# Optimization experiments

Measured on AMD Instinct MI355X. Metric: run time of the kernel, lower is better.

## Reference

```python
import jax, jax.numpy as jnp
import numpy as np
from jax import lax

B, T, C = 2, 2048, 1024
HEAD = 64          # head_size N
H = C // HEAD      # n_head
EPS_GN = 0.00064   # GroupNorm epsilon from module


def l2norm(x, eps=1e-12):
    inv = lax.rsqrt(jnp.sum(x * x, axis=-1, keepdims=True) + eps)
    return x * jnp.maximum(inv, eps)


def group_norm(x, gamma, beta, groups, eps):
    n, c = x.shape
    xg = x.reshape(n, groups, c // groups)
    mu = jnp.mean(xg, axis=-1, keepdims=True)
    var = jnp.mean(jnp.square(xg - mu), axis=-1, keepdims=True)
    xg = (xg - mu) * lax.rsqrt(var + eps)
    return xg.reshape(n, c) * gamma + beta


def rwkv7_scan(r, w, k, v, a, b):
    # all [B,T,H,N]; w is log-decay, actual per-channel decay = exp(-exp(w))
    decay = jnp.exp(-jnp.exp(w))

    def step(state, inp):  # state: [B,H,N,N] (value dim i, key dim j)
        r_t, d_t, k_t, v_t, a_t, b_t = inp  # each [B,H,N]
        sa = jnp.einsum('bhij,bhj->bhi', state, a_t)
        state = (state * d_t[:, :, None, :]
                 + sa[:, :, :, None] * b_t[:, :, None, :]
                 + v_t[:, :, :, None] * k_t[:, :, None, :])
        out = jnp.einsum('bhij,bhj->bhi', state, r_t)
        return state, out

    xs = tuple(jnp.moveaxis(t, 1, 0) for t in (r, decay, k, v, a, b))
    state0 = jnp.zeros((r.shape[0], H, HEAD, HEAD), r.dtype)
    final_state, out = lax.scan(step, state0, xs)
    return jnp.moveaxis(out, 0, 1), final_state


def setup_inputs():
    key = jax.random.key(0)
    ks = jax.random.split(key, 32)

    def p(i, shape, scale=0.02):
        return jax.random.normal(ks[i], shape, jnp.float32) * scale

    return dict(
        x=jax.random.normal(ks[0], (B, T, C), jnp.float32),
        v_first=jax.random.normal(ks[1], (B, T, C), jnp.float32),
        x_r=p(2, (1, 1, C)), x_w=p(3, (1, 1, C)), x_k=p(4, (1, 1, C)),
        x_v=p(5, (1, 1, C)), x_a=p(6, (1, 1, C)), x_g=p(7, (1, 1, C)),
        w0=p(8, (1, 1, C)), w1=p(9, (C, 64)), w2=p(10, (64, C)),
        a0=p(11, (1, 1, C)), a1=p(12, (C, 64)), a2=p(13, (64, C)),
        v0=p(14, (1, 1, C)), v1=p(15, (C, 32)), v2=p(16, (32, C)),
        g1=p(17, (C, 128)), g2=p(18, (128, C)),
        k_k=p(19, (1, 1, C), 0.5), k_a=p(20, (1, 1, C), 0.5),
        r_k=p(21, (H, HEAD), 0.5),
        Wr=p(22, (C, C)), Wk=p(23, (C, C)), Wv=p(24, (C, C)), Wo=p(25, (C, C)),
        ln_gamma=jnp.ones((C,), jnp.float32),
        ln_beta=jnp.zeros((C,), jnp.float32),
    )


def reference(x, v_first, x_r, x_w, x_k, x_v, x_a, x_g, w0, w1, w2,
              a0, a1, a2, v0, v1, v2, g1, g2, k_k, k_a, r_k,
              Wr, Wk, Wv, Wo, ln_gamma, ln_beta):
    # time_shift(x) - x
    xx = jnp.pad(x, ((0, 0), (1, 0), (0, 0)))[:, :-1] - x
    xr = x + xx * x_r
    xw = x + xx * x_w
    xk = x + xx * x_k
    xv = x + xx * x_v
    xa = x + xx * x_a
    xg = x + xx * x_g

    r = xr @ Wr
    k = xk @ Wk
    v = xv @ Wv
    w = -jax.nn.softplus(-(w0 + jnp.tanh(xw @ w1) @ w2)) - 0.5
    # v_first provided (non-first layer path)
    v = v + (v_first - v) * jax.nn.sigmoid(v0 + (xv @ v1) @ v2)
    a = jax.nn.sigmoid(a0 + (xa @ a1) @ a2)
    g = jax.nn.sigmoid(xg @ g1) @ g2

    kk = l2norm((k * k_k).reshape(B, T, H, HEAD)).reshape(B, T, C)
    k = k * (1.0 + (a - 1.0) * k_a)

    r4 = r.reshape(B, T, H, HEAD)
    y, _ = rwkv7_scan(r4,
                      w.reshape(B, T, H, HEAD),
                      k.reshape(B, T, H, HEAD),
                      v.reshape(B, T, H, HEAD),
                      (-kk).reshape(B, T, H, HEAD),
                      (kk * a).reshape(B, T, H, HEAD))

    y = group_norm(y.reshape(B * T, C), ln_gamma, ln_beta, H, EPS_GN).reshape(B, T, C)

    k4 = k.reshape(B, T, H, HEAD)
    v4 = v.reshape(B, T, H, HEAD)
    rwkv = jnp.sum(r4 * k4 * r_k, axis=-1, keepdims=True) * v4  # [B,T,H,N]
    y = y + rwkv.reshape(B, T, C)
    return (y * g) @ Wo
```

## Files before the change

### kernel.cpp

```cpp
#include <hip/hip_runtime.h>
#include <hip/hip_bf16.h>
#include <math.h>

#define TSEQ 2048
#define HEADS 16
#define HSZ 64
#define CDIM 1024
#define MROWS 4096
#define CHUNK 64
#define NCHUNK (TSEQ/CHUNK)
#define NBH 32
#define LSTR 68
#define K2 2048

typedef short bf16x8 __attribute__((ext_vector_type(8)));
typedef short bf16x4 __attribute__((ext_vector_type(4)));
typedef float f32x4 __attribute__((ext_vector_type(4)));

__device__ __forceinline__ float sigf(float x) { return 1.0f / (1.0f + expf(-x)); }

__device__ __forceinline__ short to_bf16(float f) {
    __hip_bfloat16 h = __float2bfloat16(f);
    return *reinterpret_cast<short*>(&h);
}
__device__ __forceinline__ float bf2f(short s) {
    unsigned int u = ((unsigned int)(unsigned short)s) << 16;
    return __uint_as_float(u);
}

__global__ __launch_bounds__(256)
void mix_make(const float* __restrict__ x, short* __restrict__ ax)
{
    const int m = blockIdx.x;
    const int cc = threadIdx.x * 4;
    const float4 xv = *(const float4*)(x + (size_t)m*CDIM + cc);
    float4 xp = make_float4(0.f, 0.f, 0.f, 0.f);
    if ((m & (TSEQ-1)) != 0) xp = *(const float4*)(x + (size_t)(m-1)*CDIM + cc);
    bf16x4 a, b;
    a[0] = to_bf16(xv.x); a[1] = to_bf16(xv.y);
    a[2] = to_bf16(xv.z); a[3] = to_bf16(xv.w);
    b[0] = to_bf16(xp.x - xv.x); b[1] = to_bf16(xp.y - xv.y);
    b[2] = to_bf16(xp.z - xv.z); b[3] = to_bf16(xp.w - xv.w);
    *(bf16x4*)(ax + (size_t)m*K2 + cc)        = a;
    *(bf16x4*)(ax + (size_t)m*K2 + CDIM + cc) = b;
}

__global__ __launch_bounds__(256)
void transpose_cvt(const float* __restrict__ W, short* __restrict__ Wt,
                   const int K, const int N)
{
    __shared__ float t[32][33];
    const int k0 = blockIdx.y * 32, n0 = blockIdx.x * 32;
    const int lx = threadIdx.x & 31, ly = threadIdx.x >> 5;
#pragma unroll
    for (int i = 0; i < 4; ++i)
        t[ly + i*8][lx] = W[(size_t)(k0 + ly + i*8)*N + n0 + lx];
    __syncthreads();
#pragma unroll
    for (int i = 0; i < 4; ++i)
        Wt[(size_t)(n0 + ly + i*8)*K + k0 + lx] = to_bf16(t[lx][ly + i*8]);
}

__global__ __launch_bounds__(256)
void transpose_cvt_scaled(const float* __restrict__ W, const float* __restrict__ mix,
                          short* __restrict__ Wt, const int N)
{
    __shared__ float t[32][33];
    const int k0 = blockIdx.y * 32, n0 = blockIdx.x * 32;
    const int lx = threadIdx.x & 31, ly = threadIdx.x >> 5;
#pragma unroll
    for (int i = 0; i < 4; ++i)
        t[ly + i*8][lx] = W[(size_t)(k0 + ly + i*8)*N + n0 + lx];
    __syncthreads();
    const float mv = mix[k0 + lx];
#pragma unroll
    for (int i = 0; i < 4; ++i) {
        const float w = t[lx][ly + i*8];
        short* base = Wt + (size_t)(n0 + ly + i*8)*K2 + k0 + lx;
        base[0]    = to_bf16(w);
        base[CDIM] = to_bf16(mv * w);
    }
}

template<int BN, int MODE>
__global__ __launch_bounds__(256)
void gemm_mfma(const short* __restrict__ A, const short* __restrict__ Bt,
               void* __restrict__ Cptr, const int M, const int N, const int K)
{
    constexpr int BM = 128, BK = 32;
    constexpr int ASTR = BK + 8;
    constexpr int NWC = (BN >= 128) ? 2 : 1;
    constexpr int NWR = 4 / NWC;
    constexpr int WM = BM / NWR;
    constexpr int WN = BN / NWC;
    constexpr int AM = WM / 16;
    constexpr int AN = WN / 16;

    __shared__ short As[BM * ASTR];
    __shared__ short Bs[BN * ASTR];

    const int tid  = threadIdx.x;
    const int bm   = blockIdx.y * BM;
    const int bn   = blockIdx.x * BN;
    const int wid  = tid >> 6;
    const int lane = tid & 63;
    const int wr   = wid / NWC;
    const int wc   = wid % NWC;
    const int lrow = lane & 15;
    const int koff = (lane >> 4) * 8;

    f32x4 acc[AM][AN];
#pragma unroll
    for (int m = 0; m < AM; ++m)
#pragma unroll
        for (int n = 0; n < AN; ++n)
            acc[m][n] = (f32x4){0.f, 0.f, 0.f, 0.f};

    for (int k0 = 0; k0 < K; k0 += BK) {
        __syncthreads();
#pragma unroll
        for (int p = 0; p < (BM*BK)/(256*8); ++p) {
            const int c = p*256 + tid;
            const int row = c >> 2;
            const int kc  = (c & 3) * 8;
            *(bf16x8*)&As[row*ASTR + kc] =
                *(const bf16x8*)(A + (size_t)(bm+row)*K + k0 + kc);
        }
        {
            constexpr int CHUNKS = (BN*BK)/8;
#pragma unroll
            for (int p = 0; p < (CHUNKS + 255)/256; ++p) {
                const int c = p*256 + tid;
                if ((CHUNKS & 255) == 0 || c < CHUNKS) {
                    const int col = c >> 2;
                    const int kc  = (c & 3) * 8;
                    *(bf16x8*)&Bs[col*ASTR + kc] =
                        *(const bf16x8*)(Bt + (size_t)(bn+col)*K + k0 + kc);
                }
            }
        }
        __syncthreads();

        bf16x8 af[AM], bfv[AN];
#pragma unroll
        for (int m = 0; m < AM; ++m)
            af[m] = *(const bf16x8*)&As[(wr*WM + m*16 + lrow)*ASTR + koff];
#pragma unroll
        for (int n = 0; n < AN; ++n)
            bfv[n] = *(const bf16x8*)&Bs[(wc*WN + n*16 + lrow)*ASTR + koff];
#pragma unroll
        for (int m = 0; m < AM; ++m)
#pragma unroll
            for (int n = 0; n < AN; ++n)
                acc[m][n] = __builtin_amdgcn_mfma_f32_16x16x32_bf16(
                    af[m], bfv[n], acc[m][n], 0, 0, 0);
    }

    const int r0 = (lane >> 4) * 4;
#pragma unroll
    for (int m = 0; m < AM; ++m) {
#pragma unroll
        for (int n = 0; n < AN; ++n) {
#pragma unroll
            for (int j = 0; j < 4; ++j) {
                const int row = bm + wr*WM + m*16 + r0 + j;
                const int col = bn + wc*WN + n*16 + lrow;
                float vv = acc[m][n][j];
                if (MODE == 0) {
                    ((float*)Cptr)[(size_t)row*N + col] = vv;
                } else if (MODE == 1) {
                    ((float*)Cptr)[(size_t)(col >> 10)*((size_t)MROWS*CDIM)
                                   + (size_t)row*CDIM + (col & 1023)] = vv;
                } else {
                    short* o = (short*)Cptr;
                    if (bn < 64)
                        o[(size_t)row*64 + col] = to_bf16(tanhf(vv));
                    else if (bn < 96)
                        (o + (size_t)MROWS*64)[(size_t)row*32 + col - 64] = to_bf16(vv);
                    else if (bn < 160)
                        (o + (size_t)MROWS*96)[(size_t)row*64 + col - 96] = to_bf16(vv);
                    else
                        (o + (size_t)MROWS*160)[(size_t)row*128 + col - 160] = to_bf16(sigf(vv));
                }
            }
        }
    }
}

__global__ __launch_bounds__(256)
void post_kernel(const float* __restrict__ tw, const float* __restrict__ vv,
                 const float* __restrict__ aa,
                 const float* __restrict__ w0, const float* __restrict__ v0p,
                 const float* __restrict__ a0p,
                 const float* __restrict__ k_k, const float* __restrict__ k_a,
                 const float* __restrict__ vfirst,
                 float* __restrict__ kio, float* __restrict__ vio,
                 float* __restrict__ dout, float* __restrict__ kkout,
                 float* __restrict__ bout)
{
    const int m  = blockIdx.x;
    const int c4 = threadIdx.x;
    const size_t o4 = (size_t)m*256 + c4;
    const int cc = c4*4;

    const float4 twv = ((const float4*)tw)[o4];
    const float4 vvv = ((const float4*)vv)[o4];
    const float4 aav = ((const float4*)aa)[o4];
    const float4 kv  = ((const float4*)kio)[o4];
    const float4 vv0 = ((const float4*)vio)[o4];
    const float4 vfv = ((const float4*)vfirst)[o4];
    const float4 w0v = *(const float4*)(w0 + cc);
    const float4 v0v = *(const float4*)(v0p + cc);
    const float4 a0v = *(const float4*)(a0p + cc);
    const float4 kkc = *(const float4*)(k_k + cc);
    const float4 kac = *(const float4*)(k_a + cc);

    float dec[4], vnew[4], av[4], kkr[4], knew[4];
    const float tws[4] = {twv.x, twv.y, twv.z, twv.w};
    const float vvs[4] = {vvv.x, vvv.y, vvv.z, vvv.w};
    const float aas[4] = {aav.x, aav.y, aav.z, aav.w};
    const float ks[4]  = {kv.x, kv.y, kv.z, kv.w};
    const float vs[4]  = {vv0.x, vv0.y, vv0.z, vv0.w};
    const float vfs[4] = {vfv.x, vfv.y, vfv.z, vfv.w};
    const float w0s[4] = {w0v.x, w0v.y, w0v.z, w0v.w};
    const float v0s[4] = {v0v.x, v0v.y, v0v.z, v0v.w};
    const float a0s[4] = {a0v.x, a0v.y, a0v.z, a0v.w};
    const float kks[4] = {kkc.x, kkc.y, kkc.z, kkc.w};
    const float kas[4] = {kac.x, kac.y, kac.z, kac.w};

    float ss = 0.f;
#pragma unroll
    for (int i = 0; i < 4; ++i) {
        dec[i]  = expf(-0.6065306597126334f * sigf(w0s[i] + tws[i]));
        const float sv = sigf(v0s[i] + vvs[i]);
        vnew[i] = vs[i] + (vfs[i] - vs[i]) * sv;
        av[i]   = sigf(a0s[i] + aas[i]);
        kkr[i]  = ks[i] * kks[i];
        knew[i] = ks[i] * (1.f + (av[i] - 1.f) * kas[i]);
        ss = fmaf(kkr[i], kkr[i], ss);
    }
#pragma unroll
    for (int mask = 1; mask < 16; mask <<= 1) ss += __shfl_xor(ss, mask);
    const float inv = fmaxf(rsqrtf(ss + 1e-12f), 1e-12f);

    float4 decv, vnv, knv, kkv4, bv4;
    decv.x = dec[0]; decv.y = dec[1]; decv.z = dec[2]; decv.w = dec[3];
    vnv.x = vnew[0]; vnv.y = vnew[1]; vnv.z = vnew[2]; vnv.w = vnew[3];
    knv.x = knew[0]; knv.y = knew[1]; knv.z = knew[2]; knv.w = knew[3];
    kkv4.x = kkr[0]*inv; kkv4.y = kkr[1]*inv; kkv4.z = kkr[2]*inv; kkv4.w = kkr[3]*inv;
    bv4.x = kkv4.x*av[0]; bv4.y = kkv4.y*av[1]; bv4.z = kkv4.z*av[2]; bv4.w = kkv4.w*av[3];

    ((float4*)dout)[o4]  = decv;
    ((float4*)vio)[o4]   = vnv;
    ((float4*)kio)[o4]   = knv;
    ((float4*)kkout)[o4] = kkv4;
    ((float4*)bout)[o4]  = bv4;
}

__device__ __forceinline__ void zero4(f32x4 a[4]) {
#pragma unroll
    for (int n = 0; n < 4; ++n) a[n] = (f32x4){0.f, 0.f, 0.f, 0.f};
}

__device__ __forceinline__ void mm_nt_w(const short* __restrict__ Ab,
                                        const short* __restrict__ Bb,
                                        f32x4 acc[4], const int lane, const int woff)
{
    const int lrow = lane & 15;
    const int ko   = (lane >> 4) * 8;
#pragma unroll
    for (int kh = 0; kh < 2; ++kh) {
        const bf16x8 af = *(const bf16x8*)&Ab[(woff + lrow)*LSTR + kh*32 + ko];
        bf16x8 bv[4];
#pragma unroll
        for (int n = 0; n < 4; ++n)
            bv[n] = *(const bf16x8*)&Bb[(n*16 + lrow)*LSTR + kh*32 + ko];
#pragma unroll
        for (int n = 0; n < 4; ++n)
            acc[n] = __builtin_amdgcn_mfma_f32_16x16x32_bf16(af, bv[n], acc[n], 0, 0, 0);
    }
}

__device__ __forceinline__ void mm_nt_gf32_w(const short* __restrict__ Ab,
                                             const float* __restrict__ Bg,
                                             f32x4 acc[4], const int lane, const int woff)
{
    const int lrow = lane & 15;
    const int ko   = (lane >> 4) * 8;
#pragma unroll
    for (int kh = 0; kh < 2; ++kh) {
        const bf16x8 af = *(const bf16x8*)&Ab[(woff + lrow)*LSTR + kh*32 + ko];
#pragma unroll
        for (int n = 0; n < 4; ++n) {
            const float* p = Bg + (size_t)(n*16 + lrow)*64 + kh*32 + ko;
            const float4 u0 = *(const float4*)p;
            const float4 u1 = *(const float4*)(p + 4);
            bf16x8 bv;
            bv[0] = to_bf16(u0.x); bv[1] = to_bf16(u0.y);
            bv[2] = to_bf16(u0.z); bv[3] = to_bf16(u0.w);
            bv[4] = to_bf16(u1.x); bv[5] = to_bf16(u1.y);
            bv[6] = to_bf16(u1.z); bv[7] = to_bf16(u1.w);
            acc[n] = __builtin_amdgcn_mfma_f32_16x16x32_bf16(af, bv, acc[n], 0, 0, 0);
        }
    }
}

template<int MASK, bool WRN, bool WRT>
__device__ __forceinline__ void acc_store_w(const f32x4 acc[4],
                                            short* __restrict__ dst,
                                            short* __restrict__ dstT,
                                            const int lane, const int woff)
{
    const int r0 = (lane >> 4) * 4;
    const int c0 = lane & 15;
#pragma unroll
    for (int n = 0; n < 4; ++n)
#pragma unroll
        for (int j = 0; j < 4; ++j) {
            const int row = woff + r0 + j;
            const int col = n*16 + c0;
            float vv = acc[n][j];
            if (MASK == 1 && col >= row) vv = 0.f;
            if (MASK == 2 && col >  row) vv = 0.f;
            const short bv = to_bf16(vv);
            if (WRN) dst [row*LSTR + col] = bv;
            if (WRT) dstT[col*LSTR + row] = bv;
        }
}

__device__ __forceinline__ void acc_init_lds_w(f32x4 acc[4],
                                               const short* __restrict__ src,
                                               const int lane, const int woff)
{
    const int r0 = (lane >> 4) * 4;
    const int c0 = lane & 15;
#pragma unroll
    for (int n = 0; n < 4; ++n)
#pragma unroll
        for (int j = 0; j < 4; ++j)
            acc[n][j] = bf2f(src[(woff + r0 + j)*LSTR + n*16 + c0]);
}

__device__ __forceinline__ void acc_init_glb_w(f32x4 acc[4],
                                               const short* __restrict__ src,
                                               const int lane, const int woff)
{
    const int r0 = (lane >> 4) * 4;
    const int c0 = lane & 15;
#pragma unroll
    for (int n = 0; n < 4; ++n)
#pragma unroll
        for (int j = 0; j < 4; ++j)
            acc[n][j] = bf2f(src[(woff + r0 + j)*64 + n*16 + c0]);
}

__global__ __launch_bounds__(256)
void scan_pass1_wy(const float* __restrict__ d, const float* __restrict__ k,
                   const float* __restrict__ v, const float* __restrict__ kk,
                   const float* __restrict__ bb,
                   float* __restrict__ Gbuf, float* __restrict__ Hbuf,
                   short* __restrict__ Yg, short* __restrict__ Ug)
{
    __shared__ short L[8*64*LSTR];
    __shared__ float wsum[4][64];
    __shared__ float cTl[64];
    short* A_  = L + 0*64*LSTR;
    short* B_  = L + 1*64*LSTR;
    short* K_  = L + 2*64*LSTR;
    short* V_  = L + 3*64*LSTR;
    short* BT_ = L + 4*64*LSTR;
    short* KT_ = L + 5*64*LSTR;
    short* N_  = L + 6*64*LSTR;
    short* NT_ = L + 7*64*LSTR;

    const int chunk = blockIdx.x;
    const int bh = blockIdx.y;
    const int b = bh >> 4, h = bh & 15;
    const int tid = threadIdx.x;
    const int w = tid >> 6;
    const int lane = tid & 63;
    const int woff = w * 16;

    const size_t base = ((size_t)b*TSEQ + (size_t)chunk*CHUNK + woff)*CDIM + h*HSZ + lane;
    float lc[16];
    float s = 0.f;
#pragma unroll
    for (int t = 0; t < 16; ++t) { s += logf(d[base + (size_t)t*CDIM]); lc[t] = s; }
    wsum[w][lane] = s;
    __syncthreads();
    float pre = 0.f;
#pragma unroll
    for (int w2 = 0; w2 < 3; ++w2) if (w2 < w) pre += wsum[w2][lane];
    if (w == 3) cTl[lane] = expf(pre + s);

#pragma unroll
    for (int t = 0; t < 16; ++t) {
        const int tg = woff + t;
        const size_t off = base + (size_t)t*CDIM;
        const float run   = pre + lc[t];
        const float cprev = (t == 0) ? pre : (pre + lc[t-1]);
        const float ern   = expf(-run);
        A_[tg*LSTR + lane] = to_bf16(-kk[off] * expf(cprev));
        const short bv = to_bf16(bb[off] * ern);
        B_[tg*LSTR + lane] = bv;  BT_[lane*LSTR + tg] = bv;
        const short kv = to_bf16(k[off] * ern);
        K_[tg*LSTR + lane] = kv;  KT_[lane*LSTR + tg] = kv;
        V_[lane*LSTR + tg] = to_bf16(v[off]);
    }
    __syncthreads();

    f32x4 xj[4], xi[4], tmp[4];

    zero4(tmp);  mm_nt_w(A_, B_, tmp, lane, woff);
    acc_init_lds_w(xj, A_, lane, woff);
    acc_store_w<1, true, true>(tmp, N_, NT_, lane, woff);
    __syncthreads();

    acc_store_w<0, false, true>(xj, nullptr, B_, lane, woff);
    zero4(tmp);  mm_nt_w(A_, K_, tmp, lane, woff);
    __syncthreads();
    acc_store_w<1, true, false>(tmp, K_, nullptr, lane, woff);
    __syncthreads();

    zero4(xi);  mm_nt_w(K_, V_, xi, lane, woff);
    acc_store_w<0, false, true>(xi, nullptr, A_, lane, woff);
    __syncthreads();

#pragma unroll 1
    for (int rd = 0; rd < 6; ++rd) {
        mm_nt_w(N_, B_, xj, lane, woff);
        mm_nt_w(N_, A_, xi, lane, woff);
        if (rd < 5) { zero4(tmp); mm_nt_w(N_, NT_, tmp, lane, woff); }
        __syncthreads();
        acc_store_w<0, false, true>(xj, nullptr, B_, lane, woff);
        acc_store_w<0, false, true>(xi, nullptr, A_, lane, woff);
        if (rd < 5) acc_store_w<0, true, true>(tmp, N_, NT_, lane, woff);
        __syncthreads();
    }

    const size_t mb = ((size_t)bh*NCHUNK + chunk)*HSZ*HSZ;
    const int r0 = (lane >> 4) * 4;
    const int c0 = lane & 15;

#pragma unroll
    for (int n = 0; n < 4; ++n)
#pragma unroll
        for (int j = 0; j < 4; ++j) {
            const int row = woff + r0 + j;
            const int col = n*16 + c0;
            Yg[mb + row*64 + col] = to_bf16(xj[n][j]);
            Ug[mb + row*64 + col] = to_bf16(xi[n][j]);
        }

    float ctv[4];
#pragma unroll
    for (int n = 0; n < 4; ++n) ctv[n] = cTl[n*16 + c0];

    zero4(tmp);  mm_nt_w(B_, BT_, tmp, lane, woff);
#pragma unroll
    for (int n = 0; n < 4; ++n)
#pragma unroll
        for (int j = 0; j < 4; ++j) {
            const int row = woff + r0 + j;
            const int col = n*16 + c0;
            const float id = (row == col) ? 1.f : 0.f;
            Gbuf[mb + (size_t)row*HSZ + col] = (tmp[n][j] + id) * ctv[n];
        }

    zero4(tmp);
    mm_nt_w(A_, BT_, tmp, lane, woff);
    mm_nt_w(V_, KT_, tmp, lane, woff);
#pragma unroll
    for (int n = 0; n < 4; ++n)
#pragma unroll
        for (int j = 0; j < 4; ++j) {
            const int row = woff + r0 + j;
            const int col = n*16 + c0;
            Hbuf[mb + (size_t)row*HSZ + col] = tmp[n][j] * ctv[n];
        }
}

__global__ __launch_bounds__(256)
void scan_pass2(const float* __restrict__ Gbuf, const float* __restrict__ Hbuf,
                float* __restrict__ S0buf)
{
    const int rg = blockIdx.x;
    const int bh = blockIdx.y;
    const int tid = threadIdx.x;
    const int il = tid & 15;
    const int q4 = tid >> 4;
    const int row = rg*16 + il;

    __shared__ float Gs[64][68];
    __shared__ float Ssh[16][68];

    float frag[4] = {0.f, 0.f, 0.f, 0.f};
    *(float4*)&Ssh[il][q4*4] = make_float4(0.f, 0.f, 0.f, 0.f);

    for (int c = 0; c < NCHUNK; ++c) {
        const size_t mbase = ((size_t)bh*NCHUNK + c)*HSZ*HSZ;
#pragma unroll
        for (int p = 0; p < 4; ++p) {
            const int f = tid*16 + p*4;
            const int rr = f >> 6, cc = f & 63;
            *(float4*)&Gs[rr][cc] = *(const float4*)(Gbuf + mbase + f);
        }
        *(float4*)(S0buf + mbase + (size_t)row*HSZ + q4*4) =
            make_float4(frag[0], frag[1], frag[2], frag[3]);
        __syncthreads();

        float4 hv = *(const float4*)(Hbuf + mbase + (size_t)row*HSZ + q4*4);
        float a0 = hv.x, a1 = hv.y, a2 = hv.z, a3 = hv.w;
#pragma unroll
        for (int j = 0; j < 64; ++j) {
            const float sj = Ssh[il][j];
            const float4 gv = *(const float4*)&Gs[j][q4*4];
            a0 = fmaf(sj, gv.x, a0);
            a1 = fmaf(sj, gv.y, a1);
            a2 = fmaf(sj, gv.z, a2);
            a3 = fmaf(sj, gv.w, a3);
        }
        __syncthreads();
        frag[0] = a0; frag[1] = a1; frag[2] = a2; frag[3] = a3;
        *(float4*)&Ssh[il][q4*4] = make_float4(a0, a1, a2, a3);
    }
}

__global__ __launch_bounds__(256)
void scan_pass3_lite4(const float* __restrict__ r, const float* __restrict__ d,
                      const float* __restrict__ k, const float* __restrict__ v,
                      const float* __restrict__ bb,
                      const short* __restrict__ Yg, const short* __restrict__ Ug,
                      const float* __restrict__ S0buf, float* __restrict__ y)
{
    __shared__ short L[8*64*LSTR];
    __shared__ float wsum[4][64];
    short* R_  = L + 0*64*LSTR;
    short* B_  = L + 1*64*LSTR;
    short* K_  = L + 2*64*LSTR;
    short* V_  = L + 3*64*LSTR;
    short* Yn  = L + 4*64*LSTR;
    short* Wt  = L + 5*64*LSTR;
    short* P1b = L + 6*64*LSTR;
    short* P2b = L + 7*64*LSTR;

    const int chunk = blockIdx.x;
    const int bh = blockIdx.y;
    const int b = bh >> 4, h = bh & 15;
    const int tid = threadIdx.x;
    const int w = tid >> 6;
    const int lane = tid & 63;
    const int woff = w * 16;
    const size_t mb = ((size_t)bh*NCHUNK + chunk)*HSZ*HSZ;

    const size_t base = ((size_t)b*TSEQ + (size_t)chunk*CHUNK + woff)*CDIM + h*HSZ + lane;
    float lc[16];
    float s = 0.f;
#pragma unroll
    for (int t = 0; t < 16; ++t) { s += logf(d[base + (size_t)t*CDIM]); lc[t] = s; }
    wsum[w][lane] = s;
    __syncthreads();
    float pre = 0.f;
#pragma unroll
    for (int w2 = 0; w2 < 3; ++w2) if (w2 < w) pre += wsum[w2][lane];

#pragma unroll
    for (int t = 0; t < 16; ++t) {
        const int tg = woff + t;
        const size_t off = base + (size_t)t*CDIM;
        const float run = pre + lc[t];
        const float ern = expf(-run);
        R_[tg*LSTR + lane] = to_bf16(r[off] * expf(run));
        B_[tg*LSTR + lane] = to_bf16(bb[off] * ern);
        K_[tg*LSTR + lane] = to_bf16(k[off]  * ern);
        V_[lane*LSTR + tg] = to_bf16(v[off]);
    }
    {
        const int row = woff + (lane & 15);
        const int cb  = (lane >> 4) * 16;
        const short* yp = Yg + mb + (size_t)row*64 + cb;
        *(bf16x8*)&Yn[row*LSTR + cb]     = *(const bf16x8*)yp;
        *(bf16x8*)&Yn[row*LSTR + cb + 8] = *(const bf16x8*)(yp + 8);
    }
    __syncthreads();

    const float* S0g = S0buf + mb;
    f32x4 a4[4], o4[4];

    acc_init_glb_w(a4, Ug + mb, lane, woff);
    mm_nt_gf32_w(Yn, S0g, a4, lane, woff);
    acc_store_w<0, false, true>(a4, nullptr, Wt, lane, woff);

    zero4(a4);  mm_nt_w(R_, B_, a4, lane, woff);
    acc_store_w<2, true, false>(a4, P1b, nullptr, lane, woff);
    zero4(a4);  mm_nt_w(R_, K_, a4, lane, woff);
    acc_store_w<2, true, false>(a4, P2b, nullptr, lane, woff);
    __syncthreads();

    zero4(o4);
    mm_nt_gf32_w(R_, S0g, o4, lane, woff);
    mm_nt_w(P1b, Wt, o4, lane, woff);
    mm_nt_w(P2b, V_, o4, lane, woff);

    const int r0 = (lane >> 4) * 4;
    const int c0 = lane & 15;
    float* yb = y + ((size_t)b*TSEQ + (size_t)chunk*CHUNK)*CDIM + h*HSZ;
#pragma unroll
    for (int n = 0; n < 4; ++n)
#pragma unroll
        for (int j = 0; j < 4; ++j)
            yb[(size_t)(woff + r0 + j)*CDIM + n*16 + c0] = o4[n][j];
}

__global__ __launch_bounds__(1024)
void gn_kernel(const float* __restrict__ r, const float* __restrict__ k,
               const float* __restrict__ v, const float* __restrict__ g,
               const float* __restrict__ rk, const float* __restrict__ gamma,
               const float* __restrict__ beta, const float* __restrict__ y,
               short* __restrict__ ybf)
{
    const int m = blockIdx.x;
    const int c = threadIdx.x;
    const size_t o = (size_t)m*CDIM + c;
    const float yv = y[o];
    float s1 = yv, s2 = yv*yv;
#pragma unroll
    for (int mask = 1; mask < 64; mask <<= 1) {
        s1 += __shfl_xor(s1, mask);
        s2 += __shfl_xor(s2, mask);
    }
    const float mu  = s1 * (1.f/HSZ);
    const float var = s2 * (1.f/HSZ) - mu*mu;
    const float gn  = (yv - mu) * rsqrtf(var + 0.00064f) * gamma[c] + beta[c];

    float p = r[o] * k[o] * rk[c];
#pragma unroll
    for (int mask = 1; mask < 64; mask <<= 1) p += __shfl_xor(p, mask);

    ybf[o] = to_bf16((gn + p * v[o]) * g[o]);
}

extern "C" void kernel_launch(void* const* d_in, const int* in_sizes, int n_in,
                              void* d_out, int out_size, void* d_ws, size_t ws_size,
                              hipStream_t stream)
{
    const float* x      = (const float*)d_in[0];
    const float* vfirst = (const float*)d_in[1];
    const float* x_r = (const float*)d_in[2];
    const float* x_w = (const float*)d_in[3];
    const float* x_k = (const float*)d_in[4];
    const float* x_v = (const float*)d_in[5];
    const float* x_a = (const float*)d_in[6];
    const float* x_g = (const float*)d_in[7];
    const float* w0  = (const float*)d_in[8];
    const float* w1  = (const float*)d_in[9];
    const float* w2  = (const float*)d_in[10];
    const float* a0  = (const float*)d_in[11];
    const float* a1  = (const float*)d_in[12];
    const float* a2  = (const float*)d_in[13];
    const float* v0p = (const float*)d_in[14];
    const float* v1  = (const float*)d_in[15];
    const float* v2  = (const float*)d_in[16];
    const float* g1  = (const float*)d_in[17];
    const float* g2  = (const float*)d_in[18];
    const float* k_k = (const float*)d_in[19];
    const float* k_a = (const float*)d_in[20];
    const float* r_k = (const float*)d_in[21];
    const float* Wr  = (const float*)d_in[22];
    const float* Wk  = (const float*)d_in[23];
    const float* Wv  = (const float*)d_in[24];
    const float* Wo  = (const float*)d_in[25];
    const float* lng = (const float*)d_in[26];
    const float* lnb = (const float*)d_in[27];
    float* outp = (float*)d_out;

    float* ws = (float*)d_ws;
    const size_t BIG = (size_t)MROWS * CDIM;
    float* rbuf  = ws + 0*BIG;
    float* kbuf  = ws + 1*BIG;
    float* vbuf  = ws + 2*BIG;
    float* dbuf  = ws + 3*BIG;
    float* kkbuf = ws + 4*BIG;
    float* bbuf  = ws + 5*BIG;
    float* gbuf  = ws + 6*BIG;
    float* ybuf  = ws + 7*BIG;
    float* smbuf = ws + 8*BIG;
    short* hwbf  = (short*)smbuf;
    short* wT    = (short*)(smbuf + (size_t)MROWS*160/2);
    short* Brkv = wT;
    short* Bsm  = Brkv + (size_t)3072*K2;
    short* WoT  = Bsm  + (size_t)288*K2;
    short* g2T  = WoT  + (size_t)CDIM*CDIM;
    short* w2T  = g2T  + (size_t)CDIM*128;
    short* v2T  = w2T  + (size_t)CDIM*64;
    short* a2T  = v2T  + (size_t)CDIM*32;
    short* axbf = a2T  + (size_t)CDIM*64;

    short* Yg = axbf;
    short* Ug = axbf + (size_t)NBH*NCHUNK*HSZ*HSZ;

    float* twbuf = ybuf;
    float* vvbuf = gbuf;
    float* aabuf = outp;

    float* Gbuf  = ybuf;
    float* Hbuf  = gbuf;
    float* S0buf = outp;
    short* ybf   = (short*)dbuf;
    short* ghbf  = hwbf + (size_t)MROWS*160;

    const dim3 blk(256);

    mix_make<<<dim3(MROWS), blk, 0, stream>>>(x, axbf);
    transpose_cvt_scaled<<<dim3(CDIM/32, CDIM/32), blk, 0, stream>>>(Wr, x_r, Brkv, CDIM);
    transpose_cvt_scaled<<<dim3(CDIM/32, CDIM/32), blk, 0, stream>>>(Wk, x_k, Brkv + (size_t)1024*K2, CDIM);
    transpose_cvt_scaled<<<dim3(CDIM/32, CDIM/32), blk, 0, stream>>>(Wv, x_v, Brkv + (size_t)2048*K2, CDIM);
    transpose_cvt_scaled<<<dim3(64/32,   CDIM/32), blk, 0, stream>>>(w1, x_w, Bsm, 64);
    transpose_cvt_scaled<<<dim3(32/32,   CDIM/32), blk, 0, stream>>>(v1, x_v, Bsm + (size_t)64*K2, 32);
    transpose_cvt_scaled<<<dim3(64/32,   CDIM/32), blk, 0, stream>>>(a1, x_a, Bsm + (size_t)96*K2, 64);
    transpose_cvt_scaled<<<dim3(128/32,  CDIM/32), blk, 0, stream>>>(g1, x_g, Bsm + (size_t)160*K2, 128);
    transpose_cvt<<<dim3(CDIM/32, CDIM/32), blk, 0, stream>>>(Wo, WoT, CDIM, CDIM);
    transpose_cvt<<<dim3(CDIM/32, 128/32),  blk, 0, stream>>>(g2, g2T, 128, CDIM);
    transpose_cvt<<<dim3(CDIM/32, 64/32),   blk, 0, stream>>>(w2, w2T, 64, CDIM);
    transpose_cvt<<<dim3(CDIM/32, 32/32),   blk, 0, stream>>>(v2, v2T, 32, CDIM);
    transpose_cvt<<<dim3(CDIM/32, 64/32),   blk, 0, stream>>>(a2, a2T, 64, CDIM);

    gemm_mfma<128,1><<<dim3(3072/128, MROWS/128), blk, 0, stream>>>(
        axbf, Brkv, rbuf, MROWS, 3072, K2);
    gemm_mfma<32,2><<<dim3(288/32, MROWS/128), blk, 0, stream>>>(
        axbf, Bsm, hwbf, MROWS, 288, K2);
    gemm_mfma<128,0><<<dim3(CDIM/128, MROWS/128), blk, 0, stream>>>(
        hwbf, w2T, twbuf, MROWS, CDIM, 64);
    gemm_mfma<128,0><<<dim3(CDIM/128, MROWS/128), blk, 0, stream>>>(
        hwbf + (size_t)MROWS*64, v2T, vvbuf, MROWS, CDIM, 32);
    gemm_mfma<128,0><<<dim3(CDIM/128, MROWS/128), blk, 0, stream>>>(
        hwbf + (size_t)MROWS*96, a2T, aabuf, MROWS, CDIM, 64);

    post_kernel<<<dim3(MROWS), blk, 0, stream>>>(
        twbuf, vvbuf, aabuf, w0, v0p, a0, k_k, k_a, vfirst,
        kbuf, vbuf, dbuf, kkbuf, bbuf);

    scan_pass1_wy<<<dim3(NCHUNK, NBH), blk, 0, stream>>>(
        dbuf, kbuf, vbuf, kkbuf, bbuf, Gbuf, Hbuf, Yg, Ug);
    scan_pass2<<<dim3(4, NBH), blk, 0, stream>>>(Gbuf, Hbuf, S0buf);
    scan_pass3_lite4<<<dim3(NCHUNK, NBH), blk, 0, stream>>>(
        rbuf, dbuf, kbuf, vbuf, bbuf, Yg, Ug, S0buf, ybuf);

    gemm_mfma<128,0><<<dim3(CDIM/128, MROWS/128), blk, 0, stream>>>(
        ghbf, g2T, gbuf, MROWS, CDIM, 128);

    gn_kernel<<<dim3(MROWS), dim3(1024), 0, stream>>>(
        rbuf, kbuf, vbuf, gbuf, r_k, lng, lnb, ybuf, ybf);

    gemm_mfma<128,0><<<dim3(CDIM/128, MROWS/128), blk, 0, stream>>>(
        ybf, WoT, outp, MROWS, CDIM, CDIM);
}
```

Before: 469.0 us.

## Split scan pass1 across eight waves and use direct decay products

The WY-factor kernel for scan pass 1 now runs with 512 threads. Each wave computes a 16x32 quarter-tile instead of a 16x64 tile, which doubles the waves available to hide MFMA and LDS latency. Both scan kernels replace the log-sum/exp cumulative decay with running products and reciprocals, removing the logf and expf calls. The risk is float underflow or overflow of the products over a 64-step chunk when decays are small, where the log-domain form was safer.

```diff
diff --git a/kernel.cpp b/kernel.cpp
--- a/kernel.cpp
+++ b/kernel.cpp
@@ -328,19 +328,6 @@
         }
 }
 
-__device__ __forceinline__ void acc_init_lds_w(f32x4 acc[4],
-                                               const short* __restrict__ src,
-                                               const int lane, const int woff)
-{
-    const int r0 = (lane >> 4) * 4;
-    const int c0 = lane & 15;
-#pragma unroll
-    for (int n = 0; n < 4; ++n)
-#pragma unroll
-        for (int j = 0; j < 4; ++j)
-            acc[n][j] = bf2f(src[(woff + r0 + j)*LSTR + n*16 + c0]);
-}
-
 __device__ __forceinline__ void acc_init_glb_w(f32x4 acc[4],
                                                const short* __restrict__ src,
                                                const int lane, const int woff)
@@ -354,7 +341,68 @@
             acc[n][j] = bf2f(src[(woff + r0 + j)*64 + n*16 + c0]);
 }
 
-__global__ __launch_bounds__(256)
+__device__ __forceinline__ void zero2(f32x4 a[2]) {
+    a[0] = (f32x4){0.f, 0.f, 0.f, 0.f};
+    a[1] = (f32x4){0.f, 0.f, 0.f, 0.f};
+}
+
+__device__ __forceinline__ void mm_nt_q(const short* __restrict__ Ab,
+                                        const short* __restrict__ Bb,
+                                        f32x4 acc[2], const int lane,
+                                        const int woff, const int noff)
+{
+    const int lrow = lane & 15;
+    const int ko   = (lane >> 4) * 8;
+#pragma unroll
+    for (int kh = 0; kh < 2; ++kh) {
+        const bf16x8 af = *(const bf16x8*)&Ab[(woff + lrow)*LSTR + kh*32 + ko];
+#pragma unroll
+        for (int n = 0; n < 2; ++n) {
+            const bf16x8 bv = *(const bf16x8*)&Bb[(noff + n*16 + lrow)*LSTR + kh*32 + ko];
+            acc[n] = __builtin_amdgcn_mfma_f32_16x16x32_bf16(af, bv, acc[n], 0, 0, 0);
+        }
+    }
+}
+
+template<int MASK, bool WRN, bool WRT>
+__device__ __forceinline__ void acc_store_q(const f32x4 acc[2],
+                                            short* __restrict__ dst,
+                                            short* __restrict__ dstT,
+                                            const int lane,
+                                            const int woff, const int noff)
+{
+    const int r0 = (lane >> 4) * 4;
+    const int c0 = lane & 15;
+#pragma unroll
+    for (int n = 0; n < 2; ++n)
+#pragma unroll
+        for (int j = 0; j < 4; ++j) {
+            const int row = woff + r0 + j;
+            const int col = noff + n*16 + c0;
+            float vv = acc[n][j];
+            if (MASK == 1 && col >= row) vv = 0.f;
+            if (MASK == 2 && col >  row) vv = 0.f;
+            const short bv = to_bf16(vv);
+            if (WRN) dst [row*LSTR + col] = bv;
+            if (WRT) dstT[col*LSTR + row] = bv;
+        }
+}
+
+__device__ __forceinline__ void acc_init_lds_q(f32x4 acc[2],
+                                               const short* __restrict__ src,
+                                               const int lane,
+                                               const int woff, const int noff)
+{
+    const int r0 = (lane >> 4) * 4;
+    const int c0 = lane & 15;
+#pragma unroll
+    for (int n = 0; n < 2; ++n)
+#pragma unroll
+        for (int j = 0; j < 4; ++j)
+            acc[n][j] = bf2f(src[(woff + r0 + j)*LSTR + noff + n*16 + c0]);
+}
+
+__global__ __launch_bounds__(512)
 void scan_pass1_wy(const float* __restrict__ d, const float* __restrict__ k,
                    const float* __restrict__ v, const float* __restrict__ kk,
                    const float* __restrict__ bb,
@@ -362,7 +410,7 @@
                    short* __restrict__ Yg, short* __restrict__ Ug)
 {
     __shared__ short L[8*64*LSTR];
-    __shared__ float wsum[4][64];
+    __shared__ float wprod[8][64];
     __shared__ float cTl[64];
     short* A_  = L + 0*64*LSTR;
     short* B_  = L + 1*64*LSTR;
@@ -379,28 +427,29 @@
     const int tid = threadIdx.x;
     const int w = tid >> 6;
     const int lane = tid & 63;
-    const int woff = w * 16;
-
-    const size_t base = ((size_t)b*TSEQ + (size_t)chunk*CHUNK + woff)*CDIM + h*HSZ + lane;
-    float lc[16];
-    float s = 0.f;
-#pragma unroll
-    for (int t = 0; t < 16; ++t) { s += logf(d[base + (size_t)t*CDIM]); lc[t] = s; }
-    wsum[w][lane] = s;
-    __syncthreads();
-    float pre = 0.f;
-#pragma unroll
-    for (int w2 = 0; w2 < 3; ++w2) if (w2 < w) pre += wsum[w2][lane];
-    if (w == 3) cTl[lane] = expf(pre + s);
-
-#pragma unroll
-    for (int t = 0; t < 16; ++t) {
-        const int tg = woff + t;
+    const int woff = (w >> 1) * 16;
+    const int noff = (w & 1) * 32;
+
+    const size_t base = ((size_t)b*TSEQ + (size_t)chunk*CHUNK + w*8)*CDIM + h*HSZ + lane;
+    float lc[8];
+    float s = 1.f;
+#pragma unroll
+    for (int t = 0; t < 8; ++t) { s *= d[base + (size_t)t*CDIM]; lc[t] = s; }
+    wprod[w][lane] = s;
+    __syncthreads();
+    float pre = 1.f;
+#pragma unroll
+    for (int w2 = 0; w2 < 7; ++w2) if (w2 < w) pre *= wprod[w2][lane];
+    if (w == 7) cTl[lane] = pre * s;
+
+#pragma unroll
+    for (int t = 0; t < 8; ++t) {
+        const int tg = w*8 + t;
         const size_t off = base + (size_t)t*CDIM;
-        const float run   = pre + lc[t];
-        const float cprev = (t == 0) ? pre : (pre + lc[t-1]);
-        const float ern   = expf(-run);
-        A_[tg*LSTR + lane] = to_bf16(-kk[off] * expf(cprev));
+        const float run   = pre * lc[t];
+        const float cprev = (t == 0) ? pre : (pre * lc[t-1]);
+        const float ern   = 1.f / run;
+        A_[tg*LSTR + lane] = to_bf16(-kk[off] * cprev);
         const short bv = to_bf16(bb[off] * ern);
         B_[tg*LSTR + lane] = bv;  BT_[lane*LSTR + tg] = bv;
         const short kv = to_bf16(k[off] * ern);
@@ -409,32 +458,32 @@
     }
     __syncthreads();
 
-    f32x4 xj[4], xi[4], tmp[4];
-
-    zero4(tmp);  mm_nt_w(A_, B_, tmp, lane, woff);
-    acc_init_lds_w(xj, A_, lane, woff);
-    acc_store_w<1, true, true>(tmp, N_, NT_, lane, woff);
-    __syncthreads();
-
-    acc_store_w<0, false, true>(xj, nullptr, B_, lane, woff);
-    zero4(tmp);  mm_nt_w(A_, K_, tmp, lane, woff);
-    __syncthreads();
-    acc_store_w<1, true, false>(tmp, K_, nullptr, lane, woff);
-    __syncthreads();
-
-    zero4(xi);  mm_nt_w(K_, V_, xi, lane, woff);
-    acc_store_w<0, false, true>(xi, nullptr, A_, lane, woff);
+    f32x4 xj[2], xi[2], tmp[2];
+
+    zero2(tmp);  mm_nt_q(A_, B_, tmp, lane, woff, noff);
+    acc_init_lds_q(xj, A_, lane, woff, noff);
+    acc_store_q<1, true, true>(tmp, N_, NT_, lane, woff, noff);
+    __syncthreads();
+
+    acc_store_q<0, false, true>(xj, nullptr, B_, lane, woff, noff);
+    zero2(tmp);  mm_nt_q(A_, K_, tmp, lane, woff, noff);
+    __syncthreads();
+    acc_store_q<1, true, false>(tmp, K_, nullptr, lane, woff, noff);
+    __syncthreads();
+
+    zero2(xi);  mm_nt_q(K_, V_, xi, lane, woff, noff);
+    acc_store_q<0, false, true>(xi, nullptr, A_, lane, woff, noff);
     __syncthreads();
 
 #pragma unroll 1
     for (int rd = 0; rd < 6; ++rd) {
-        mm_nt_w(N_, B_, xj, lane, woff);
-        mm_nt_w(N_, A_, xi, lane, woff);
-        if (rd < 5) { zero4(tmp); mm_nt_w(N_, NT_, tmp, lane, woff); }
+        mm_nt_q(N_, B_, xj, lane, woff, noff);
+        mm_nt_q(N_, A_, xi, lane, woff, noff);
+        if (rd < 5) { zero2(tmp); mm_nt_q(N_, NT_, tmp, lane, woff, noff); }
         __syncthreads();
-        acc_store_w<0, false, true>(xj, nullptr, B_, lane, woff);
-        acc_store_w<0, false, true>(xi, nullptr, A_, lane, woff);
-        if (rd < 5) acc_store_w<0, true, true>(tmp, N_, NT_, lane, woff);
+        acc_store_q<0, false, true>(xj, nullptr, B_, lane, woff, noff);
+        acc_store_q<0, false, true>(xi, nullptr, A_, lane, woff, noff);
+        if (rd < 5) acc_store_q<0, true, true>(tmp, N_, NT_, lane, woff, noff);
         __syncthreads();
     }
 
@@ -443,39 +492,39 @@
     const int c0 = lane & 15;
 
 #pragma unroll
-    for (int n = 0; n < 4; ++n)
+    for (int n = 0; n < 2; ++n)
 #pragma unroll
         for (int j = 0; j < 4; ++j) {
             const int row = woff + r0 + j;
-            const int col = n*16 + c0;
+            const int col = noff + n*16 + c0;
             Yg[mb + row*64 + col] = to_bf16(xj[n][j]);
             Ug[mb + row*64 + col] = to_bf16(xi[n][j]);
         }
 
-    float ctv[4];
-#pragma unroll
-    for (int n = 0; n < 4; ++n) ctv[n] = cTl[n*16 + c0];
-
-    zero4(tmp);  mm_nt_w(B_, BT_, tmp, lane, woff);
-#pragma unroll
-    for (int n = 0; n < 4; ++n)
+    float ctv[2];
+#pragma unroll
+    for (int n = 0; n < 2; ++n) ctv[n] = cTl[noff + n*16 + c0];
+
+    zero2(tmp);  mm_nt_q(B_, BT_, tmp, lane, woff, noff);
+#pragma unroll
+    for (int n = 0; n < 2; ++n)
 #pragma unroll
         for (int j = 0; j < 4; ++j) {
             const int row = woff + r0 + j;
-            const int col = n*16 + c0;
+            const int col = noff + n*16 + c0;
             const float id = (row == col) ? 1.f : 0.f;
             Gbuf[mb + (size_t)row*HSZ + col] = (tmp[n][j] + id) * ctv[n];
         }
 
-    zero4(tmp);
-    mm_nt_w(A_, BT_, tmp, lane, woff);
-    mm_nt_w(V_, KT_, tmp, lane, woff);
-#pragma unroll
-    for (int n = 0; n < 4; ++n)
+    zero2(tmp);
+    mm_nt_q(A_, BT_, tmp, lane, woff, noff);
+    mm_nt_q(V_, KT_, tmp, lane, woff, noff);
+#pragma unroll
+    for (int n = 0; n < 2; ++n)
 #pragma unroll
         for (int j = 0; j < 4; ++j) {
             const int row = woff + r0 + j;
-            const int col = n*16 + c0;
+            const int col = noff + n*16 + c0;
             Hbuf[mb + (size_t)row*HSZ + col] = tmp[n][j] * ctv[n];
         }
 }
@@ -534,7 +583,7 @@
                       const float* __restrict__ S0buf, float* __restrict__ y)
 {
     __shared__ short L[8*64*LSTR];
-    __shared__ float wsum[4][64];
+    __shared__ float wprod[4][64];
     short* R_  = L + 0*64*LSTR;
     short* B_  = L + 1*64*LSTR;
     short* K_  = L + 2*64*LSTR;
@@ -555,22 +604,22 @@
 
     const size_t base = ((size_t)b*TSEQ + (size_t)chunk*CHUNK + woff)*CDIM + h*HSZ + lane;
     float lc[16];
-    float s = 0.f;
-#pragma unroll
-    for (int t = 0; t < 16; ++t) { s += logf(d[base + (size_t)t*CDIM]); lc[t] = s; }
-    wsum[w][lane] = s;
-    __syncthreads();
-    float pre = 0.f;
-#pragma unroll
-    for (int w2 = 0; w2 < 3; ++w2) if (w2 < w) pre += wsum[w2][lane];
+    float s = 1.f;
+#pragma unroll
+    for (int t = 0; t < 16; ++t) { s *= d[base + (size_t)t*CDIM]; lc[t] = s; }
+    wprod[w][lane] = s;
+    __syncthreads();
+    float pre = 1.f;
+#pragma unroll
+    for (int w2 = 0; w2 < 3; ++w2) if (w2 < w) pre *= wprod[w2][lane];
 
 #pragma unroll
     for (int t = 0; t < 16; ++t) {
         const int tg = woff + t;
         const size_t off = base + (size_t)t*CDIM;
-        const float run = pre + lc[t];
-        const float ern = expf(-run);
-        R_[tg*LSTR + lane] = to_bf16(r[off] * expf(run));
+        const float run = pre * lc[t];
+        const float ern = 1.f / run;
+        R_[tg*LSTR + lane] = to_bf16(r[off] * run);
         B_[tg*LSTR + lane] = to_bf16(bb[off] * ern);
         K_[tg*LSTR + lane] = to_bf16(k[off]  * ern);
         V_[lane*LSTR + tg] = to_bf16(v[off]);
@@ -740,7 +789,7 @@
         twbuf, vvbuf, aabuf, w0, v0p, a0, k_k, k_a, vfirst,
         kbuf, vbuf, dbuf, kkbuf, bbuf);
 
-    scan_pass1_wy<<<dim3(NCHUNK, NBH), blk, 0, stream>>>(
+    scan_pass1_wy<<<dim3(NCHUNK, NBH), dim3(512), 0, stream>>>(
         dbuf, kbuf, vbuf, kkbuf, bbuf, Gbuf, Hbuf, Yg, Ug);
     scan_pass2<<<dim3(4, NBH), blk, 0, stream>>>(Gbuf, Hbuf, S0buf);
     scan_pass3_lite4<<<dim3(NCHUNK, NBH), blk, 0, stream>>>(
```

After: 477.6 us. No clear change (+1.8%).
